# Kernel optimization log

Measured on AMD Instinct MI355X. Metric: run time of the kernel, lower is better.

The kernel has to match this reference:

```python
import jax, jax.numpy as jnp
import numpy as np

ROT = 0.785  # rotation_factor


def _apply_1q(state, U, w):
    # state: (N,2,2,2,2) complex; apply 2x2 U on wire w
    s = jnp.moveaxis(state, w + 1, -1)
    s = jnp.einsum('...a,ba->...b', s, U)
    return jnp.moveaxis(s, -1, w + 1)


def _rz_batched(state, theta, w):
    # per-sample RZ(theta) on wire w; theta: (N,)
    half = theta * 0.5
    ph = jnp.stack([jnp.cos(half) - 1j * jnp.sin(half),
                    jnp.cos(half) + 1j * jnp.sin(half)], axis=-1)  # (N,2)
    s = jnp.moveaxis(state, w + 1, -1)
    s = s * ph.reshape(ph.shape[0], 1, 1, 1, 2)
    return jnp.moveaxis(s, -1, w + 1)


def _cnot(state, c, t):
    s = jnp.moveaxis(state, (c + 1, t + 1), (1, 2))  # (N,2,2,...)
    s = jnp.concatenate([s[:, :1], jnp.flip(s[:, 1:2], axis=2)], axis=1)
    return jnp.moveaxis(s, (1, 2), (c + 1, t + 1))


def _circuit(x, w):
    # x: (N,4) patch pixel values, w: (4,) RX angles. Returns (N,4) Z expectations [Z3,Z2,Z1,Z0].
    N = x.shape[0]
    state = jnp.zeros((N, 2, 2, 2, 2), jnp.complex64).at[:, 0, 0, 0, 0].set(1.0)
    H = jnp.asarray(np.array([[1, 1], [1, -1]], np.complex64) / np.sqrt(2).astype(np.float32))
    # feature encoding: H + RZ(x_i * 0.785)
    for q in range(4):
        state = _apply_1q(state, H, q)
        state = _rz_batched(state, x[:, q] * ROT, q)
    # pairwise feature products: CNOT - RZ(x_i*x_j*0.785) - CNOT
    for i in range(3):
        for j in range(i + 1, 4):
            theta = x[:, i] * x[:, j] * ROT
            state = _cnot(state, i, j)
            state = _rz_batched(state, theta, j)
            state = _cnot(state, i, j)
    # RX(weights[0][q]) layer (shared angles)
    for q in range(4):
        c = jnp.cos(w[q] * 0.5)
        s_ = jnp.sin(w[q] * 0.5)
        RX = jnp.stack([jnp.stack([c + 0j, -1j * s_]),
                        jnp.stack([-1j * s_, c + 0j])]).astype(jnp.complex64)
        state = _apply_1q(state, RX, q)
    # entangling CNOT chain + closing ring
    for q in range(3):
        state = _cnot(state, q, q + 1)
    state = _cnot(state, 3, 0)
    probs = state.real ** 2 + state.imag ** 2  # (N,2,2,2,2)
    ez = []
    for q in range(4):
        p = jnp.moveaxis(probs, q + 1, 1).reshape(N, 2, -1).sum(-1)  # (N,2)
        ez.append(p[:, 0] - p[:, 1])
    # observable order in source: [obs_3, obs_2, obs_1, obs_0]
    return jnp.stack([ez[3], ez[2], ez[1], ez[0]], axis=-1)


def setup_inputs() -> dict:
    key = jax.random.key(0)
    k1, k2 = jax.random.split(key)
    image = jax.random.uniform(k1, (4096, 1, 28, 28), dtype=jnp.float32)
    weights = jax.random.normal(k2, (1, 4), dtype=jnp.float32)
    return {"image": image, "weights": weights}


def reference(image, weights):
    B = image.shape[0]
    # extract 2x2 patches: x0=[j,k], x1=[j,k+1], x2=[j+1,k], x3=[j+1,k+1]
    patches = image[:, 0].reshape(B, 14, 2, 14, 2).transpose(0, 1, 3, 2, 4).reshape(B * 196, 4)
    out = _circuit(patches, weights[0])  # (B*196, 4)
    return out.reshape(B, 14, 14, 4).transpose(0, 3, 1, 2)  # (B,4,14,14)
```

## Files before the change

### kernel.cpp

```cpp
#include <hip/hip_runtime.h>


#define NPATCH (4096 * 196)

__global__ __launch_bounds__(256) void qconv_kernel(
    const float* __restrict__ img,
    const float* __restrict__ w,
    float* __restrict__ out)
{
    int p = blockIdx.x * blockDim.x + threadIdx.x;
    if (p >= NPATCH) return;

    int b   = p / 196;
    int rem = p - b * 196;
    int r   = rem / 14;
    int c   = rem - r * 14;

    const float2* row0 = (const float2*)(img + b * 784 + (2 * r) * 28 + 2 * c);
    const float2* row1 = (const float2*)(img + b * 784 + (2 * r + 1) * 28 + 2 * c);
    float2 p0 = row0[0];
    float2 p1 = row1[0];
    float x0 = p0.x, x1 = p0.y, x2 = p1.x, x3 = p1.y;

    const float HR = 0.3925f;
    float t0 = x0 * HR, t1 = x1 * HR, t2 = x2 * HR, t3 = x3 * HR;
    float u01 = x0 * x1 * HR, u02 = x0 * x2 * HR, u03 = x0 * x3 * HR;
    float u12 = x1 * x2 * HR, u13 = x1 * x3 * HR, u23 = x2 * x3 * HR;

    float sr[16], si[16];
#pragma unroll
    for (int k = 0; k < 16; ++k) {
        const int b0 = (k >> 3) & 1, b1 = (k >> 2) & 1, b2 = (k >> 1) & 1, b3 = k & 1;
        float phi = (b0 ? t0 : -t0) + (b1 ? t1 : -t1) + (b2 ? t2 : -t2) + (b3 ? t3 : -t3)
                  + ((b0 ^ b1) ? u01 : -u01) + ((b0 ^ b2) ? u02 : -u02)
                  + ((b0 ^ b3) ? u03 : -u03) + ((b1 ^ b2) ? u12 : -u12)
                  + ((b1 ^ b3) ? u13 : -u13) + ((b2 ^ b3) ? u23 : -u23);
        float sn, cs;
        __sincosf(phi, &sn, &cs);
        sr[k] = 0.25f * cs;
        si[k] = 0.25f * sn;
    }

    float w0 = w[0], w1 = w[1], w2 = w[2], w3 = w[3];
#pragma unroll
    for (int q = 0; q < 4; ++q) {
        float wq = (q == 0) ? w0 : (q == 1) ? w1 : (q == 2) ? w2 : w3;
        float sq, cq;
        __sincosf(0.5f * wq, &sq, &cq);
        const int stride = 8 >> q;
#pragma unroll
        for (int k = 0; k < 16; ++k) {
            if (k & stride) continue;
            const int k1 = k | stride;
            float a0r = sr[k], a0i = si[k];
            float a1r = sr[k1], a1i = si[k1];
            sr[k]  = cq * a0r + sq * a1i;
            si[k]  = cq * a0i - sq * a1r;
            sr[k1] = cq * a1r + sq * a0i;
            si[k1] = cq * a1i - sq * a0r;
        }
    }

    float e0 = 0.f, e1 = 0.f, e2 = 0.f, e3 = 0.f;
#pragma unroll
    for (int k = 0; k < 16; ++k) {
        const int b0 = (k >> 3) & 1, b1 = (k >> 2) & 1, b2 = (k >> 1) & 1, b3 = k & 1;
        float pk = sr[k] * sr[k] + si[k] * si[k];
        e0 += ((b1 ^ b2 ^ b3) ? -pk : pk);
        e1 += ((b0 ^ b1) ? -pk : pk);
        e2 += ((b0 ^ b1 ^ b2) ? -pk : pk);
        e3 += ((b0 ^ b1 ^ b2 ^ b3) ? -pk : pk);
    }

    float* o = out + b * (4 * 196) + r * 14 + c;
    o[0 * 196] = e3;
    o[1 * 196] = e2;
    o[2 * 196] = e1;
    o[3 * 196] = e0;
}

extern "C" void kernel_launch(void* const* d_in, const int* in_sizes, int n_in,
                              void* d_out, int out_size, void* d_ws, size_t ws_size,
                              hipStream_t stream) {
    const float* img = (const float*)d_in[0];
    const float* w   = (const float*)d_in[1];
    float* out       = (float*)d_out;

    const int threads = 256;
    const int blocks  = (NPATCH + threads - 1) / threads;
    qconv_kernel<<<blocks, threads, 0, stream>>>(img, w, out);
}
```

Before: 76.52 us.

## Pack amplitudes into float2 vectors, use hardware sin/cos, and fold scaling

Restructures the 16-amplitude state as 8 two-wide vectors paired on qubit 0, so the later RX gates and the reductions can use packed FP32 math. Phase computation shares partial sums between each pair. The 0.25 amplitude scale moves into a single final 0.0625 factor. __sincosf is replaced by the raw amdgcn sin/cos builtins on pre-scaled arguments. The bounds check and grid rounding are dropped because NPATCH divides evenly by 256. The raw builtins give up range reduction, which is acceptable for the small phases here.

```diff
diff --git a/kernel.cpp b/kernel.cpp
--- a/kernel.cpp
+++ b/kernel.cpp
@@ -1,76 +1,108 @@
 #include <hip/hip_runtime.h>
 
 
+typedef float v2f __attribute__((ext_vector_type(2)));
+
 #define NPATCH (4096 * 196)
+#define INV2PI 0.15915494309189535f
+
+__device__ __forceinline__ void fast_sincos(float x, float* s, float* c) {
+    float r = x * INV2PI;
+    *s = __builtin_amdgcn_sinf(r);
+    *c = __builtin_amdgcn_cosf(r);
+}
 
 __global__ __launch_bounds__(256) void qconv_kernel(
     const float* __restrict__ img,
     const float* __restrict__ w,
     float* __restrict__ out)
 {
-    int p = blockIdx.x * blockDim.x + threadIdx.x;
-    if (p >= NPATCH) return;
+    const int p = blockIdx.x * blockDim.x + threadIdx.x;
 
-    int b   = p / 196;
-    int rem = p - b * 196;
-    int r   = rem / 14;
-    int c   = rem - r * 14;
+    const int b   = p / 196;
+    const int rem = p - b * 196;
+    const int r   = rem / 14;
+    const int c   = rem - r * 14;
 
     const float2* row0 = (const float2*)(img + b * 784 + (2 * r) * 28 + 2 * c);
     const float2* row1 = (const float2*)(img + b * 784 + (2 * r + 1) * 28 + 2 * c);
-    float2 p0 = row0[0];
-    float2 p1 = row1[0];
-    float x0 = p0.x, x1 = p0.y, x2 = p1.x, x3 = p1.y;
+    const float2 p0 = row0[0];
+    const float2 p1 = row1[0];
+    const float x0 = p0.x, x1 = p0.y, x2 = p1.x, x3 = p1.y;
 
     const float HR = 0.3925f;
-    float t0 = x0 * HR, t1 = x1 * HR, t2 = x2 * HR, t3 = x3 * HR;
-    float u01 = x0 * x1 * HR, u02 = x0 * x2 * HR, u03 = x0 * x3 * HR;
-    float u12 = x1 * x2 * HR, u13 = x1 * x3 * HR, u23 = x2 * x3 * HR;
+    const float t0 = x0 * HR, t1 = x1 * HR, t2 = x2 * HR, t3 = x3 * HR;
+    const float u01 = x0 * x1 * HR, u02 = x0 * x2 * HR, u03 = x0 * x3 * HR;
+    const float u12 = x1 * x2 * HR, u13 = x1 * x3 * HR, u23 = x2 * x3 * HR;
 
-    float sr[16], si[16];
+    v2f srv[8], siv[8];
 #pragma unroll
-    for (int k = 0; k < 16; ++k) {
-        const int b0 = (k >> 3) & 1, b1 = (k >> 2) & 1, b2 = (k >> 1) & 1, b3 = k & 1;
-        float phi = (b0 ? t0 : -t0) + (b1 ? t1 : -t1) + (b2 ? t2 : -t2) + (b3 ? t3 : -t3)
-                  + ((b0 ^ b1) ? u01 : -u01) + ((b0 ^ b2) ? u02 : -u02)
-                  + ((b0 ^ b3) ? u03 : -u03) + ((b1 ^ b2) ? u12 : -u12)
-                  + ((b1 ^ b3) ? u13 : -u13) + ((b2 ^ b3) ? u23 : -u23);
-        float sn, cs;
-        __sincosf(phi, &sn, &cs);
-        sr[k] = 0.25f * cs;
-        si[k] = 0.25f * sn;
+    for (int m = 0; m < 8; ++m) {
+        const int b1 = (m >> 2) & 1, b2 = (m >> 1) & 1, b3 = m & 1;
+        const float G = (b1 ? u01 : -u01) + (b2 ? u02 : -u02) + (b3 ? u03 : -u03);
+        const float K = ((b1 ^ b2) ? u12 : -u12) + ((b1 ^ b3) ? u13 : -u13)
+                      + ((b2 ^ b3) ? u23 : -u23);
+        const float L = (b1 ? t1 : -t1) + (b2 ? t2 : -t2) + (b3 ? t3 : -t3);
+        const float phi0 = -t0 + L + G + K;
+        const float phi1 = phi0 + 2.0f * (t0 - G);
+        float s0, c0, s1, c1;
+        fast_sincos(phi0, &s0, &c0);
+        fast_sincos(phi1, &s1, &c1);
+        srv[m].x = c0; srv[m].y = c1;
+        siv[m].x = s0; siv[m].y = s1;
     }
 
-    float w0 = w[0], w1 = w[1], w2 = w[2], w3 = w[3];
+    const float w0 = w[0], w1 = w[1], w2 = w[2], w3 = w[3];
+
+    {
+        float sq, cq;
+        fast_sincos(0.5f * w0, &sq, &cq);
 #pragma unroll
-    for (int q = 0; q < 4; ++q) {
-        float wq = (q == 0) ? w0 : (q == 1) ? w1 : (q == 2) ? w2 : w3;
-        float sq, cq;
-        __sincosf(0.5f * wq, &sq, &cq);
-        const int stride = 8 >> q;
-#pragma unroll
-        for (int k = 0; k < 16; ++k) {
-            if (k & stride) continue;
-            const int k1 = k | stride;
-            float a0r = sr[k], a0i = si[k];
-            float a1r = sr[k1], a1i = si[k1];
-            sr[k]  = cq * a0r + sq * a1i;
-            si[k]  = cq * a0i - sq * a1r;
-            sr[k1] = cq * a1r + sq * a0i;
-            si[k1] = cq * a1i - sq * a0r;
+        for (int m = 0; m < 8; ++m) {
+            const float a0r = srv[m].x, a0i = siv[m].x;
+            const float a1r = srv[m].y, a1i = siv[m].y;
+            srv[m].x = cq * a0r + sq * a1i;
+            siv[m].x = cq * a0i - sq * a1r;
+            srv[m].y = cq * a1r + sq * a0i;
+            siv[m].y = cq * a1i - sq * a0r;
         }
     }
 
-    float e0 = 0.f, e1 = 0.f, e2 = 0.f, e3 = 0.f;
 #pragma unroll
-    for (int k = 0; k < 16; ++k) {
-        const int b0 = (k >> 3) & 1, b1 = (k >> 2) & 1, b2 = (k >> 1) & 1, b3 = k & 1;
-        float pk = sr[k] * sr[k] + si[k] * si[k];
-        e0 += ((b1 ^ b2 ^ b3) ? -pk : pk);
-        e1 += ((b0 ^ b1) ? -pk : pk);
-        e2 += ((b0 ^ b1 ^ b2) ? -pk : pk);
-        e3 += ((b0 ^ b1 ^ b2 ^ b3) ? -pk : pk);
+    for (int q = 1; q < 4; ++q) {
+        const float wq = (q == 1) ? w1 : (q == 2) ? w2 : w3;
+        float sq, cq;
+        fast_sincos(0.5f * wq, &sq, &cq);
+        const int stride = 8 >> q;
+#pragma unroll
+        for (int m = 0; m < 8; ++m) {
+            if (m & stride) continue;
+            const int m1 = m | stride;
+            const v2f A0r = srv[m], A0i = siv[m];
+            const v2f A1r = srv[m1], A1i = siv[m1];
+            srv[m]  = cq * A0r + sq * A1i;
+            siv[m]  = cq * A0i - sq * A1r;
+            srv[m1] = cq * A1r + sq * A0i;
+            siv[m1] = cq * A1i - sq * A0r;
+        }
     }
+
+    v2f ta = {0.f, 0.f};
+    v2f tb = {0.f, 0.f};
+    v2f tc = {0.f, 0.f};
+#pragma unroll
+    for (int m = 0; m < 8; ++m) {
+        const int b1 = (m >> 2) & 1, b2 = (m >> 1) & 1, b3 = m & 1;
+        const v2f pv = srv[m] * srv[m] + siv[m] * siv[m];
+        ta += (b1 ? -pv : pv);
+        tb += ((b1 ^ b2) ? -pv : pv);
+        tc += ((b1 ^ b2 ^ b3) ? -pv : pv);
+    }
+    const float SC = 0.0625f;
+    const float e0 = (tc.x + tc.y) * SC;
+    const float e1 = (ta.x - ta.y) * SC;
+    const float e2 = (tb.x - tb.y) * SC;
+    const float e3 = (tc.x - tc.y) * SC;
 
     float* o = out + b * (4 * 196) + r * 14 + c;
     o[0 * 196] = e3;
@@ -87,6 +119,6 @@
     float* out       = (float*)d_out;
 
     const int threads = 256;
-    const int blocks  = (NPATCH + threads - 1) / threads;
+    const int blocks  = NPATCH / threads;
     qconv_kernel<<<blocks, threads, 0, stream>>>(img, w, out);
 }
```

Result: faster. 73.74 us (-3.6%).
